# Kernel tuning notes

Measured on AMD Instinct MI355X. Metric: run time of the kernel, lower is better.

Reference implementation:

```python
import jax, jax.numpy as jnp
import numpy as np

SLOPE = 25.0  # snntorch fast_sigmoid default surrogate slope

@jax.custom_vjp
def spike(u):
    return (u > 0).astype(u.dtype)

def _spike_fwd(u):
    return spike(u), u

def _spike_bwd(u, g):
    return (g / (1.0 + SLOPE * jnp.abs(u)) ** 2,)

spike.defvjp(_spike_fwd, _spike_bwd)

def fake_quant(W):
    # brevitas-style int8 per-tensor symmetric fake-quant with STE
    s = jnp.max(jnp.abs(W)) / 127.0
    q = jnp.clip(jnp.round(W / s), -127.0, 127.0) * s
    return W + jax.lax.stop_gradient(q - W)

def setup_inputs() -> dict:
    key = jax.random.key(0)
    ks = jax.random.split(key, 8)
    B, NIN, T = 256, 512, 256
    H1, H2, OUT = 512, 512, 128
    data = jax.random.normal(ks[0], (B, NIN, T), dtype=jnp.float32)
    W1 = jax.random.normal(ks[1], (H1, NIN), dtype=jnp.float32) / np.sqrt(NIN)
    W2 = jax.random.normal(ks[2], (H2, H1), dtype=jnp.float32) / np.sqrt(H1)
    Wrec = jax.random.normal(ks[3], (H2, H2), dtype=jnp.float32) / np.sqrt(H2)
    W3 = jax.random.normal(ks[4], (OUT, H2), dtype=jnp.float32) / np.sqrt(H2)
    beta = jnp.float32(0.9)
    th = jnp.float32(1.0)
    return {"data": data, "W1": W1, "W2": W2, "Wrec": Wrec, "W3": W3,
            "beta1": beta, "th1": th, "beta_r": beta, "th_r": th,
            "beta2": beta, "th2": th}

def reference(data, W1, W2, Wrec, W3, beta1, th1, beta_r, th_r, beta2, th2):
    B = data.shape[0]
    H1, H2, OUT = W1.shape[0], W2.shape[0], W3.shape[0]
    W1q = fake_quant(W1)
    W2q = fake_quant(W2)
    Wrq = fake_quant(Wrec)
    W3q = fake_quant(W3)
    b1 = jnp.clip(beta1, 0.0, 1.0)
    br = jnp.clip(beta_r, 0.0, 1.0)
    b2 = jnp.clip(beta2, 0.0, 1.0)
    # time-major input: [T, B, NIN]
    xs = jnp.transpose(data, (2, 0, 1))

    def step(carry, x):
        m1, mr, sr, m2 = carry
        # leaky1: reset zero, reset_delay=False
        m1 = b1 * m1 + x @ W1q.T
        s1 = spike(m1 - th1)
        m1 = m1 * (1.0 - s1)
        # recurrent LIF (RLeaky-like), reset zero, reset_delay=True:
        # previous spike resets the membrane at the start of this step
        h = s1 @ W2q.T + sr @ Wrq.T
        mr = (br * mr + h) * (1.0 - sr)
        sr = spike(mr - th_r)
        # leaky2: reset zero, reset_delay=False
        m2 = b2 * m2 + sr @ W3q.T
        s2 = spike(m2 - th2)
        m2 = m2 * (1.0 - s2)
        return (m1, mr, sr, m2), s2

    init = (jnp.zeros((B, H1), jnp.float32),
            jnp.zeros((B, H2), jnp.float32),
            jnp.zeros((B, H2), jnp.float32),
            jnp.zeros((B, OUT), jnp.float32))
    _, spk_rec = jax.lax.scan(step, init, xs)
    return spk_rec  # [T, B, OUT]
```

## Files before the change

### kernel.cpp

```cpp
#include <hip/hip_runtime.h>

#define B_   256
#define NIN_ 512
#define T_   256
#define H1_  512
#define H2_  512
#define OUT_ 128

typedef __attribute__((ext_vector_type(8))) short bf16x8;
typedef __attribute__((ext_vector_type(4))) float f32x4;
typedef __attribute__((address_space(1))) const unsigned int* gl_cu;
typedef __attribute__((address_space(3))) unsigned int* ls_u;

__global__ void absmax_k(const float* __restrict__ W1, const float* __restrict__ W2,
                         const float* __restrict__ Wr, const float* __restrict__ W3,
                         float* __restrict__ scales) {
  const float* W; int n;
  switch (blockIdx.x) {
    case 0:  W = W1; n = H1_ * NIN_; break;
    case 1:  W = W2; n = H2_ * H1_;  break;
    case 2:  W = Wr; n = H2_ * H2_;  break;
    default: W = W3; n = OUT_ * H2_; break;
  }
  int tid = threadIdx.x;
  float m = 0.f;
  const float4* W4 = (const float4*)W;
  int n4 = n >> 2;
  for (int i = tid; i < n4; i += 256) {
    float4 v = W4[i];
    m = fmaxf(m, fmaxf(fmaxf(fabsf(v.x), fabsf(v.y)), fmaxf(fabsf(v.z), fabsf(v.w))));
  }
  __shared__ float red[256];
  red[tid] = m;
  __syncthreads();
  for (int s = 128; s > 0; s >>= 1) {
    if (tid < s) red[tid] = fmaxf(red[tid], red[tid + s]);
    __syncthreads();
  }
  if (tid == 0) scales[blockIdx.x] = red[0] / 127.0f;
}

__global__ void quant_w1t_k(const float* __restrict__ W1, const float* __restrict__ scales,
                            float* __restrict__ W1qT) {
  int idx = blockIdx.x * 256 + threadIdx.x;
  int h = idx & (H1_ - 1);
  int i = idx >> 9;
  float s = scales[0];
  float q = rintf(W1[h * NIN_ + i] / s);
  q = fminf(fmaxf(q, -127.f), 127.f);
  W1qT[idx] = q * s;
}

__global__ void quant_t_k(const float* __restrict__ W, const float* __restrict__ scales, int si,
                          signed char* __restrict__ WT, int rows, int cols) {
  int idx = blockIdx.x * 256 + threadIdx.x;
  if (idx >= rows * cols) return;
  int r = idx / cols;
  int c = idx - r * cols;
  float s = scales[si];
  float q = rintf(W[idx] / s);
  q = fminf(fmaxf(q, -127.f), 127.f);
  WT[(size_t)c * rows + r] = (signed char)q;
}

__global__ void quant_bf_k(const float* __restrict__ W, const float* __restrict__ scales,
                           int si, ushort* __restrict__ out, int n) {
  int idx = blockIdx.x * 256 + threadIdx.x;
  if (idx >= n) return;
  float s = scales[si];
  float q = rintf(W[idx] / s);
  q = fminf(fmaxf(q, -127.f), 127.f);
  out[idx] = (ushort)(__float_as_uint(q) >> 16);
}

__global__ __launch_bounds__(256) void gemm_cur1_k(const float* __restrict__ data,
                                                   const float* __restrict__ W1qT,
                                                   float* __restrict__ cur1) {
  const int b  = blockIdx.y;
  const int t0 = (blockIdx.x >> 2) << 7;
  const int h0 = (blockIdx.x & 3) << 7;
  const int tid = threadIdx.x;

  __shared__ float As[2][16][128];
  __shared__ float Bs[2][16][128];

  const int ty = tid >> 4, tx = tid & 15;
  const int wv = tid >> 6;
  const int ln = tid & 63;
  const int lrow = ln >> 5;
  const int lcol = ln & 31;

  float acc[8][8];
#pragma unroll
  for (int i = 0; i < 8; i++)
#pragma unroll
    for (int j = 0; j < 8; j++) acc[i][j] = 0.f;

  const float* dbase = data + (size_t)b * NIN_ * T_;

  auto issue = [&](int kb, int buf) {
#pragma unroll
    for (int j = 0; j < 2; j++) {
      const int kr = (wv << 2) + (j << 1);
      const float* ga = dbase + (size_t)(kb + kr + lrow) * T_ + t0 + (lcol << 2);
      __builtin_amdgcn_global_load_lds((gl_cu)ga, (ls_u)&As[buf][kr][0], 16, 0, 0);
      const float* gb = W1qT + (size_t)(kb + kr + lrow) * H1_ + h0 + (lcol << 2);
      __builtin_amdgcn_global_load_lds((gl_cu)gb, (ls_u)&Bs[buf][kr][0], 16, 0, 0);
    }
  };

  issue(0, 0);

  for (int p = 0; p < 32; p++) {
    const int cur = p & 1;
    __syncthreads();
    if (p < 31) issue((p + 1) << 4, cur ^ 1);
#pragma unroll
    for (int k = 0; k < 16; k++) {
      float4 A0 = *(const float4*)&As[cur][k][ty * 4];
      float4 A1 = *(const float4*)&As[cur][k][64 + ty * 4];
      float4 B0 = *(const float4*)&Bs[cur][k][tx * 4];
      float4 B1 = *(const float4*)&Bs[cur][k][64 + tx * 4];
      float a[8] = {A0.x, A0.y, A0.z, A0.w, A1.x, A1.y, A1.z, A1.w};
      float w[8] = {B0.x, B0.y, B0.z, B0.w, B1.x, B1.y, B1.z, B1.w};
#pragma unroll
      for (int i = 0; i < 8; i++)
#pragma unroll
        for (int j = 0; j < 8; j++)
          acc[i][j] = fmaf(a[i], w[j], acc[i][j]);
    }
  }

#pragma unroll
  for (int i = 0; i < 8; i++) {
    int row = (i < 4) ? (ty * 4 + i) : (64 + ty * 4 + (i - 4));
    float* op = cur1 + (size_t)(t0 + row) * (B_ * H1_) + (size_t)b * H1_ + h0;
    float4 cA = {acc[i][0], acc[i][1], acc[i][2], acc[i][3]};
    float4 cB = {acc[i][4], acc[i][5], acc[i][6], acc[i][7]};
    *(float4*)(op + tx * 4)      = cA;
    *(float4*)(op + 64 + tx * 4) = cB;
  }
}

__global__ __launch_bounds__(256) void scan1_k(const float* __restrict__ cur1,
                                               unsigned char* __restrict__ s1u,
                                               const float* __restrict__ beta1p,
                                               const float* __restrict__ th1p) {
  const int n = blockIdx.x * 256 + threadIdx.x;
  const float b1 = fminf(fmaxf(beta1p[0], 0.f), 1.f);
  const float th1 = th1p[0];
  const size_t S = (size_t)B_ * H1_;
  float m1 = 0.f;
  for (int t = 0; t < T_; t += 4) {
    float c0 = cur1[(size_t)t * S + n];
    float c1 = cur1[(size_t)(t + 1) * S + n];
    float c2 = cur1[(size_t)(t + 2) * S + n];
    float c3 = cur1[(size_t)(t + 3) * S + n];
    m1 = b1 * m1 + c0; bool s0 = m1 - th1 > 0.f; if (s0) m1 = 0.f;
    s1u[(size_t)t * S + n] = s0;
    m1 = b1 * m1 + c1; bool s1 = m1 - th1 > 0.f; if (s1) m1 = 0.f;
    s1u[(size_t)(t + 1) * S + n] = s1;
    m1 = b1 * m1 + c2; bool s2 = m1 - th1 > 0.f; if (s2) m1 = 0.f;
    s1u[(size_t)(t + 2) * S + n] = s2;
    m1 = b1 * m1 + c3; bool s3 = m1 - th1 > 0.f; if (s3) m1 = 0.f;
    s1u[(size_t)(t + 3) * S + n] = s3;
  }
}

__global__ __launch_bounds__(256) void gemm_spk_k(const unsigned char* __restrict__ A8,
                                                  const ushort* __restrict__ Bw,
                                                  float* __restrict__ C, int N) {
  __shared__ short As[128 * 72];
  __shared__ short Bs[128 * 72];
  const int tid = threadIdx.x;
  const int m0 = blockIdx.y << 7;
  const int n0 = blockIdx.x << 7;
  const int lane = tid & 63, wave = tid >> 6;
  const int quad = lane >> 4, lm = lane & 15;
  const int wm = wave << 5;

  f32x4 acc[2][8];
#pragma unroll
  for (int s = 0; s < 2; s++)
#pragma unroll
    for (int n = 0; n < 8; n++) acc[s][n] = (f32x4){0.f, 0.f, 0.f, 0.f};

  for (int kb = 0; kb < 512; kb += 64) {
    uint4 av[2], bv[4];
#pragma unroll
    for (int i = 0; i < 2; i++) {
      int ch = tid + (i << 8);
      int row = ch >> 2, offB = (ch & 3) << 4;
      av[i] = *(const uint4*)(A8 + (size_t)(m0 + row) * 512 + kb + offB);
    }
#pragma unroll
    for (int i = 0; i < 4; i++) {
      int ch = tid + (i << 8);
      int row = ch >> 3, off = (ch & 7) << 3;
      bv[i] = *(const uint4*)(Bw + (size_t)(n0 + row) * 512 + kb + off);
    }
    __syncthreads();
#pragma unroll
    for (int i = 0; i < 2; i++) {
      int ch = tid + (i << 8);
      int row = ch >> 2, offB = (ch & 3) << 4;
      unsigned u[4] = {av[i].x, av[i].y, av[i].z, av[i].w};
      unsigned d[8];
#pragma unroll
      for (int w = 0; w < 4; w++) {
        unsigned uu = u[w];
        d[2 * w]     = ((uu & 1u) | ((uu & 0x100u) << 8)) * 0x3F80u;
        d[2 * w + 1] = (((uu >> 16) & 1u) | ((uu & 0x1000000u) >> 8)) * 0x3F80u;
      }
      uint4* dst = (uint4*)&As[row * 72 + offB];
      dst[0] = make_uint4(d[0], d[1], d[2], d[3]);
      dst[1] = make_uint4(d[4], d[5], d[6], d[7]);
    }
#pragma unroll
    for (int i = 0; i < 4; i++) {
      int ch = tid + (i << 8);
      int row = ch >> 3, off = (ch & 7) << 3;
      *(uint4*)&Bs[row * 72 + off] = bv[i];
    }
    __syncthreads();
#pragma unroll
    for (int kc = 0; kc < 64; kc += 32) {
      bf16x8 af0 = *(const bf16x8*)&As[(wm + lm) * 72 + kc + quad * 8];
      bf16x8 af1 = *(const bf16x8*)&As[(wm + 16 + lm) * 72 + kc + quad * 8];
      bf16x8 bfr[8];
#pragma unroll
      for (int n = 0; n < 8; n++)
        bfr[n] = *(const bf16x8*)&Bs[((n << 4) + lm) * 72 + kc + quad * 8];
#pragma unroll
      for (int n = 0; n < 8; n++) {
        acc[0][n] = __builtin_amdgcn_mfma_f32_16x16x32_bf16(af0, bfr[n], acc[0][n], 0, 0, 0);
        acc[1][n] = __builtin_amdgcn_mfma_f32_16x16x32_bf16(af1, bfr[n], acc[1][n], 0, 0, 0);
      }
    }
    __syncthreads();
  }

#pragma unroll
  for (int s = 0; s < 2; s++)
#pragma unroll
    for (int n = 0; n < 8; n++) {
      int row = m0 + wm + (s << 4) + quad * 4;
      int col = n0 + (n << 4) + lm;
#pragma unroll
      for (int r = 0; r < 4; r++)
        C[(size_t)(row + r) * N + col] = acc[s][n][r];
    }
}

__device__ __forceinline__ void unp_add(unsigned w, int* a) {
  int iw = (int)w;
  a[0] += (iw << 24) >> 24;
  a[1] += (iw << 16) >> 24;
  a[2] += (iw << 8) >> 24;
  a[3] += iw >> 24;
}

__global__ __launch_bounds__(1024) void recurrent_k(
    const float* __restrict__ cur2a,
    const signed char* __restrict__ WrT,
    unsigned char* __restrict__ sru,
    const float* __restrict__ scales,
    const float* __restrict__ betarp, const float* __restrict__ thrp) {
  const int b = blockIdx.x;
  const int tid = threadIdx.x;
  const float s2sc = scales[1];
  const float srsc = scales[2];
  const float br = fminf(fmaxf(betarp[0], 0.f), 1.f);
  const float thr = thrp[0];

  const unsigned* WrT4 = (const unsigned*)WrT;

  __shared__ int red[8][H2_];
  __shared__ int lst[2][H2_];
  __shared__ int nc[2];

  if (tid < 2) nc[tid] = 0;
  __syncthreads();

  float mr = 0.f, sr_own = 0.f;
  const int g = tid >> 7;
  const int c = tid & 127;

  for (int t = 0; t < T_; t++) {
    const int old = t & 1, nxt = old ^ 1;
    float c2 = 0.f;
    if (tid < H2_) c2 = cur2a[((size_t)t * B_ + b) * H2_ + tid];
    if (tid == 1023) nc[nxt] = 0;
    const int n = nc[old];
    const int* L = lst[old];

    int a4[4] = {0, 0, 0, 0};
    int k = g;
    for (; k + 56 < n; k += 64) {
      int i0 = L[k],      i1 = L[k + 8],  i2 = L[k + 16], i3 = L[k + 24];
      int i4 = L[k + 32], i5 = L[k + 40], i6 = L[k + 48], i7 = L[k + 56];
      unsigned w0 = WrT4[(i0 << 7) + c], w1 = WrT4[(i1 << 7) + c];
      unsigned w2 = WrT4[(i2 << 7) + c], w3 = WrT4[(i3 << 7) + c];
      unsigned w4 = WrT4[(i4 << 7) + c], w5 = WrT4[(i5 << 7) + c];
      unsigned w6 = WrT4[(i6 << 7) + c], w7 = WrT4[(i7 << 7) + c];
      unp_add(w0, a4); unp_add(w1, a4); unp_add(w2, a4); unp_add(w3, a4);
      unp_add(w4, a4); unp_add(w5, a4); unp_add(w6, a4); unp_add(w7, a4);
    }
    for (; k + 24 < n; k += 32) {
      int i0 = L[k], i1 = L[k + 8], i2 = L[k + 16], i3 = L[k + 24];
      unsigned w0 = WrT4[(i0 << 7) + c], w1 = WrT4[(i1 << 7) + c];
      unsigned w2 = WrT4[(i2 << 7) + c], w3 = WrT4[(i3 << 7) + c];
      unp_add(w0, a4); unp_add(w1, a4); unp_add(w2, a4); unp_add(w3, a4);
    }
    for (; k < n; k += 8) unp_add(WrT4[(L[k] << 7) + c], a4);
    *(int4*)&red[g][c << 2] = make_int4(a4[0], a4[1], a4[2], a4[3]);
    __syncthreads();

    bool spike = false;
    if (tid < H2_) {
      int acc = red[0][tid] + red[1][tid] + red[2][tid] + red[3][tid]
              + red[4][tid] + red[5][tid] + red[6][tid] + red[7][tid];
      float h = s2sc * c2 + srsc * (float)acc;
      mr = (br * mr + h) * (1.f - sr_own);
      sr_own = (mr - thr > 0.f) ? 1.f : 0.f;
      sru[((size_t)t * B_ + b) * H2_ + tid] = (unsigned char)(sr_own != 0.f);
      spike = (sr_own != 0.f);
    }
    unsigned long long bm = __ballot(spike);
    if (bm != 0ull) {
      const int lane = tid & 63;
      const int ldr = (int)__ffsll((long long)bm) - 1;
      int base = 0;
      if (lane == ldr) base = atomicAdd(&nc[nxt], (int)__popcll(bm));
      base = __shfl(base, ldr);
      if (spike)
        lst[nxt][base + (int)__popcll(bm & ((1ull << lane) - 1ull))] = tid;
    }
    __syncthreads();
  }
}

__global__ __launch_bounds__(256) void scan3_k(const float* __restrict__ cur3,
                                               float* __restrict__ out,
                                               const float* __restrict__ scales,
                                               const float* __restrict__ beta2p,
                                               const float* __restrict__ th2p) {
  const int n = blockIdx.x * 256 + threadIdx.x;
  const float s3sc = scales[3];
  const float b2 = fminf(fmaxf(beta2p[0], 0.f), 1.f);
  const float th2 = th2p[0];
  const size_t S = (size_t)B_ * OUT_;
  float m2 = 0.f;
  for (int t = 0; t < T_; t += 4) {
    float v0 = cur3[(size_t)t * S + n];
    float v1 = cur3[(size_t)(t + 1) * S + n];
    float v2 = cur3[(size_t)(t + 2) * S + n];
    float v3 = cur3[(size_t)(t + 3) * S + n];
    m2 = b2 * m2 + s3sc * v0; float p0 = (m2 - th2 > 0.f) ? 1.f : 0.f; m2 *= (1.f - p0);
    out[(size_t)t * S + n] = p0;
    m2 = b2 * m2 + s3sc * v1; float p1 = (m2 - th2 > 0.f) ? 1.f : 0.f; m2 *= (1.f - p1);
    out[(size_t)(t + 1) * S + n] = p1;
    m2 = b2 * m2 + s3sc * v2; float p2 = (m2 - th2 > 0.f) ? 1.f : 0.f; m2 *= (1.f - p2);
    out[(size_t)(t + 2) * S + n] = p2;
    m2 = b2 * m2 + s3sc * v3; float p3 = (m2 - th2 > 0.f) ? 1.f : 0.f; m2 *= (1.f - p3);
    out[(size_t)(t + 3) * S + n] = p3;
  }
}

extern "C" void kernel_launch(void* const* d_in, const int* in_sizes, int n_in,
                              void* d_out, int out_size, void* d_ws, size_t ws_size,
                              hipStream_t stream) {
  const float* data  = (const float*)d_in[0];
  const float* W1    = (const float*)d_in[1];
  const float* W2    = (const float*)d_in[2];
  const float* Wr    = (const float*)d_in[3];
  const float* W3    = (const float*)d_in[4];
  const float* beta1 = (const float*)d_in[5];
  const float* th1   = (const float*)d_in[6];
  const float* betar = (const float*)d_in[7];
  const float* thr   = (const float*)d_in[8];
  const float* beta2 = (const float*)d_in[9];
  const float* th2   = (const float*)d_in[10];

  char* ws = (char*)d_ws;
  float*         scales = (float*)ws;
  float*         W1qT   = (float*)(ws + 4096);
  ushort*        W2bf   = (ushort*)(ws + 4096 + 1048576);
  ushort*        W3bf   = (ushort*)(ws + 4096 + 1048576 + 524288);
  signed char*   WrT    = (signed char*)(ws + 4096 + 1048576 + 524288 + 131072);
  float*         regA   = (float*)(ws + (size_t)4194304);
  unsigned char* regB   = (unsigned char*)(ws + (size_t)4194304 + 134217728);

  float* cur1  = regA;
  float* cur2a = regA;
  float* cur3  = regA;
  unsigned char* s1u = regB;
  unsigned char* sru = regB + (size_t)33554432;

  hipLaunchKernelGGL(absmax_k, dim3(4), dim3(256), 0, stream, W1, W2, Wr, W3, scales);
  hipLaunchKernelGGL(quant_w1t_k, dim3((H1_ * NIN_) / 256), dim3(256), 0, stream, W1, scales, W1qT);
  hipLaunchKernelGGL(quant_bf_k, dim3((H2_ * H1_) / 256), dim3(256), 0, stream, W2, scales, 1, W2bf, H2_ * H1_);
  hipLaunchKernelGGL(quant_t_k, dim3((H2_ * H2_) / 256), dim3(256), 0, stream, Wr, scales, 2, WrT, H2_, H2_);
  hipLaunchKernelGGL(quant_bf_k, dim3((OUT_ * H2_) / 256), dim3(256), 0, stream, W3, scales, 3, W3bf, OUT_ * H2_);

  hipLaunchKernelGGL(gemm_cur1_k, dim3(8, 256), dim3(256), 0, stream, data, W1qT, cur1);
  hipLaunchKernelGGL(scan1_k, dim3((B_ * H1_) / 256), dim3(256), 0, stream, cur1, s1u, beta1, th1);
  hipLaunchKernelGGL(gemm_spk_k, dim3(4, 512), dim3(256), 0, stream, s1u, W2bf, cur2a, H2_);
  hipLaunchKernelGGL(recurrent_k, dim3(256), dim3(1024), 0, stream, cur2a, WrT, sru, scales, betar, thr);
  hipLaunchKernelGGL(gemm_spk_k, dim3(1, 512), dim3(256), 0, stream, sru, W3bf, cur3, OUT_);
  hipLaunchKernelGGL(scan3_k, dim3((B_ * OUT_) / 256), dim3(256), 0, stream, cur3, (float*)d_out, scales, beta2, th2);
}
```

Baseline: 1.059 ms.

## Stage half of recurrent weights in LDS and merge quantization kernels

The recurrent kernel now copies the first 256 rows of the int8 transposed recurrent weights (128 KB) into shared memory once per block. It keeps two spike lists, low and high neuron indices, so gathers for low-index spikes read LDS and high-index spikes still read global memory. The four weight-quantization kernels are also merged into a single launch to cut launch overhead. The large LDS allocation limits each CU to one 1024-thread block and may raise bank conflicts on the gathered LDS reads.

```diff
diff --git a/kernel.cpp b/kernel.cpp
--- a/kernel.cpp
+++ b/kernel.cpp
@@ -40,37 +40,39 @@
   if (tid == 0) scales[blockIdx.x] = red[0] / 127.0f;
 }
 
-__global__ void quant_w1t_k(const float* __restrict__ W1, const float* __restrict__ scales,
-                            float* __restrict__ W1qT) {
-  int idx = blockIdx.x * 256 + threadIdx.x;
-  int h = idx & (H1_ - 1);
-  int i = idx >> 9;
-  float s = scales[0];
-  float q = rintf(W1[h * NIN_ + i] / s);
-  q = fminf(fmaxf(q, -127.f), 127.f);
-  W1qT[idx] = q * s;
-}
-
-__global__ void quant_t_k(const float* __restrict__ W, const float* __restrict__ scales, int si,
-                          signed char* __restrict__ WT, int rows, int cols) {
-  int idx = blockIdx.x * 256 + threadIdx.x;
-  if (idx >= rows * cols) return;
-  int r = idx / cols;
-  int c = idx - r * cols;
-  float s = scales[si];
-  float q = rintf(W[idx] / s);
-  q = fminf(fmaxf(q, -127.f), 127.f);
-  WT[(size_t)c * rows + r] = (signed char)q;
-}
-
-__global__ void quant_bf_k(const float* __restrict__ W, const float* __restrict__ scales,
-                           int si, ushort* __restrict__ out, int n) {
-  int idx = blockIdx.x * 256 + threadIdx.x;
-  if (idx >= n) return;
-  float s = scales[si];
-  float q = rintf(W[idx] / s);
-  q = fminf(fmaxf(q, -127.f), 127.f);
-  out[idx] = (ushort)(__float_as_uint(q) >> 16);
+__global__ void quant_all_k(const float* __restrict__ W1, const float* __restrict__ W2,
+                            const float* __restrict__ Wr, const float* __restrict__ W3,
+                            const float* __restrict__ scales,
+                            float* __restrict__ W1qT, ushort* __restrict__ W2bf,
+                            signed char* __restrict__ WrT, ushort* __restrict__ W3bf) {
+  const int blk = blockIdx.x;
+  if (blk < 1024) {
+    int idx = blk * 256 + threadIdx.x;
+    int h = idx & (H1_ - 1), i = idx >> 9;
+    float s = scales[0];
+    float q = rintf(W1[h * NIN_ + i] / s);
+    q = fminf(fmaxf(q, -127.f), 127.f);
+    W1qT[idx] = q * s;
+  } else if (blk < 2048) {
+    int idx = (blk - 1024) * 256 + threadIdx.x;
+    float s = scales[1];
+    float q = rintf(W2[idx] / s);
+    q = fminf(fmaxf(q, -127.f), 127.f);
+    W2bf[idx] = (ushort)(__float_as_uint(q) >> 16);
+  } else if (blk < 3072) {
+    int idx = (blk - 2048) * 256 + threadIdx.x;
+    int r = idx >> 9, c = idx & (H2_ - 1);
+    float s = scales[2];
+    float q = rintf(Wr[idx] / s);
+    q = fminf(fmaxf(q, -127.f), 127.f);
+    WrT[(size_t)c * H2_ + r] = (signed char)q;
+  } else {
+    int idx = (blk - 3072) * 256 + threadIdx.x;
+    float s = scales[3];
+    float q = rintf(W3[idx] / s);
+    q = fminf(fmaxf(q, -127.f), 127.f);
+    W3bf[idx] = (ushort)(__float_as_uint(q) >> 16);
+  }
 }
 
 __global__ __launch_bounds__(256) void gemm_cur1_k(const float* __restrict__ data,
@@ -275,11 +277,18 @@
 
   const unsigned* WrT4 = (const unsigned*)WrT;
 
+  __shared__ unsigned WrL[256 * 128];
   __shared__ int red[8][H2_];
-  __shared__ int lst[2][H2_];
-  __shared__ int nc[2];
-
-  if (tid < 2) nc[tid] = 0;
+  __shared__ int lstLo[2][256];
+  __shared__ int lstHi[2][256];
+  __shared__ int ncLo[2], ncHi[2];
+
+  {
+    const uint4* src = (const uint4*)WrT4;
+    uint4* dst = (uint4*)WrL;
+    for (int i = tid; i < 8192; i += 1024) dst[i] = src[i];
+  }
+  if (tid < 2) { ncLo[tid] = 0; ncHi[tid] = 0; }
   __syncthreads();
 
   float mr = 0.f, sr_own = 0.f;
@@ -290,29 +299,54 @@
     const int old = t & 1, nxt = old ^ 1;
     float c2 = 0.f;
     if (tid < H2_) c2 = cur2a[((size_t)t * B_ + b) * H2_ + tid];
-    if (tid == 1023) nc[nxt] = 0;
-    const int n = nc[old];
-    const int* L = lst[old];
+    if (tid == 1022) ncLo[nxt] = 0;
+    if (tid == 1023) ncHi[nxt] = 0;
+    const int nLo = ncLo[old];
+    const int nHi = ncHi[old];
+    const int* LLo = lstLo[old];
+    const int* LHi = lstHi[old];
 
     int a4[4] = {0, 0, 0, 0};
-    int k = g;
-    for (; k + 56 < n; k += 64) {
-      int i0 = L[k],      i1 = L[k + 8],  i2 = L[k + 16], i3 = L[k + 24];
-      int i4 = L[k + 32], i5 = L[k + 40], i6 = L[k + 48], i7 = L[k + 56];
-      unsigned w0 = WrT4[(i0 << 7) + c], w1 = WrT4[(i1 << 7) + c];
-      unsigned w2 = WrT4[(i2 << 7) + c], w3 = WrT4[(i3 << 7) + c];
-      unsigned w4 = WrT4[(i4 << 7) + c], w5 = WrT4[(i5 << 7) + c];
-      unsigned w6 = WrT4[(i6 << 7) + c], w7 = WrT4[(i7 << 7) + c];
-      unp_add(w0, a4); unp_add(w1, a4); unp_add(w2, a4); unp_add(w3, a4);
-      unp_add(w4, a4); unp_add(w5, a4); unp_add(w6, a4); unp_add(w7, a4);
-    }
-    for (; k + 24 < n; k += 32) {
-      int i0 = L[k], i1 = L[k + 8], i2 = L[k + 16], i3 = L[k + 24];
-      unsigned w0 = WrT4[(i0 << 7) + c], w1 = WrT4[(i1 << 7) + c];
-      unsigned w2 = WrT4[(i2 << 7) + c], w3 = WrT4[(i3 << 7) + c];
-      unp_add(w0, a4); unp_add(w1, a4); unp_add(w2, a4); unp_add(w3, a4);
-    }
-    for (; k < n; k += 8) unp_add(WrT4[(L[k] << 7) + c], a4);
+    {
+      int k = g;
+      for (; k + 56 < nLo; k += 64) {
+        int i0 = LLo[k],      i1 = LLo[k + 8],  i2 = LLo[k + 16], i3 = LLo[k + 24];
+        int i4 = LLo[k + 32], i5 = LLo[k + 40], i6 = LLo[k + 48], i7 = LLo[k + 56];
+        unsigned w0 = WrL[(i0 << 7) + c], w1 = WrL[(i1 << 7) + c];
+        unsigned w2 = WrL[(i2 << 7) + c], w3 = WrL[(i3 << 7) + c];
+        unsigned w4 = WrL[(i4 << 7) + c], w5 = WrL[(i5 << 7) + c];
+        unsigned w6 = WrL[(i6 << 7) + c], w7 = WrL[(i7 << 7) + c];
+        unp_add(w0, a4); unp_add(w1, a4); unp_add(w2, a4); unp_add(w3, a4);
+        unp_add(w4, a4); unp_add(w5, a4); unp_add(w6, a4); unp_add(w7, a4);
+      }
+      for (; k + 24 < nLo; k += 32) {
+        int i0 = LLo[k], i1 = LLo[k + 8], i2 = LLo[k + 16], i3 = LLo[k + 24];
+        unsigned w0 = WrL[(i0 << 7) + c], w1 = WrL[(i1 << 7) + c];
+        unsigned w2 = WrL[(i2 << 7) + c], w3 = WrL[(i3 << 7) + c];
+        unp_add(w0, a4); unp_add(w1, a4); unp_add(w2, a4); unp_add(w3, a4);
+      }
+      for (; k < nLo; k += 8) unp_add(WrL[(LLo[k] << 7) + c], a4);
+    }
+    {
+      int k = g;
+      for (; k + 56 < nHi; k += 64) {
+        int i0 = LHi[k],      i1 = LHi[k + 8],  i2 = LHi[k + 16], i3 = LHi[k + 24];
+        int i4 = LHi[k + 32], i5 = LHi[k + 40], i6 = LHi[k + 48], i7 = LHi[k + 56];
+        unsigned w0 = WrT4[(i0 << 7) + c], w1 = WrT4[(i1 << 7) + c];
+        unsigned w2 = WrT4[(i2 << 7) + c], w3 = WrT4[(i3 << 7) + c];
+        unsigned w4 = WrT4[(i4 << 7) + c], w5 = WrT4[(i5 << 7) + c];
+        unsigned w6 = WrT4[(i6 << 7) + c], w7 = WrT4[(i7 << 7) + c];
+        unp_add(w0, a4); unp_add(w1, a4); unp_add(w2, a4); unp_add(w3, a4);
+        unp_add(w4, a4); unp_add(w5, a4); unp_add(w6, a4); unp_add(w7, a4);
+      }
+      for (; k + 24 < nHi; k += 32) {
+        int i0 = LHi[k], i1 = LHi[k + 8], i2 = LHi[k + 16], i3 = LHi[k + 24];
+        unsigned w0 = WrT4[(i0 << 7) + c], w1 = WrT4[(i1 << 7) + c];
+        unsigned w2 = WrT4[(i2 << 7) + c], w3 = WrT4[(i3 << 7) + c];
+        unp_add(w0, a4); unp_add(w1, a4); unp_add(w2, a4); unp_add(w3, a4);
+      }
+      for (; k < nHi; k += 8) unp_add(WrT4[(LHi[k] << 7) + c], a4);
+    }
     *(int4*)&red[g][c << 2] = make_int4(a4[0], a4[1], a4[2], a4[3]);
     __syncthreads();
 
@@ -330,11 +364,13 @@
     if (bm != 0ull) {
       const int lane = tid & 63;
       const int ldr = (int)__ffsll((long long)bm) - 1;
+      int* cnt = (tid < 256) ? &ncLo[nxt] : &ncHi[nxt];
+      int* dst = (tid < 256) ? lstLo[nxt] : lstHi[nxt];
       int base = 0;
-      if (lane == ldr) base = atomicAdd(&nc[nxt], (int)__popcll(bm));
+      if (lane == ldr) base = atomicAdd(cnt, (int)__popcll(bm));
       base = __shfl(base, ldr);
       if (spike)
-        lst[nxt][base + (int)__popcll(bm & ((1ull << lane) - 1ull))] = tid;
+        dst[base + (int)__popcll(bm & ((1ull << lane) - 1ull))] = tid;
     }
     __syncthreads();
   }
@@ -398,10 +434,8 @@
   unsigned char* sru = regB + (size_t)33554432;
 
   hipLaunchKernelGGL(absmax_k, dim3(4), dim3(256), 0, stream, W1, W2, Wr, W3, scales);
-  hipLaunchKernelGGL(quant_w1t_k, dim3((H1_ * NIN_) / 256), dim3(256), 0, stream, W1, scales, W1qT);
-  hipLaunchKernelGGL(quant_bf_k, dim3((H2_ * H1_) / 256), dim3(256), 0, stream, W2, scales, 1, W2bf, H2_ * H1_);
-  hipLaunchKernelGGL(quant_t_k, dim3((H2_ * H2_) / 256), dim3(256), 0, stream, Wr, scales, 2, WrT, H2_, H2_);
-  hipLaunchKernelGGL(quant_bf_k, dim3((OUT_ * H2_) / 256), dim3(256), 0, stream, W3, scales, 3, W3bf, OUT_ * H2_);
+  hipLaunchKernelGGL(quant_all_k, dim3(3328), dim3(256), 0, stream,
+                     W1, W2, Wr, W3, scales, W1qT, W2bf, WrT, W3bf);
 
   hipLaunchKernelGGL(gemm_cur1_k, dim3(8, 256), dim3(256), 0, stream, data, W1qT, cur1);
   hipLaunchKernelGGL(scan1_k, dim3((B_ * H1_) / 256), dim3(256), 0, stream, cur1, s1u, beta1, th1);
```

New measurement: 1.030 ms. 2.7% less time.
